# Optimization experiments

Measured on AMD Instinct MI355X. Metric: run time of the kernel, lower is better.

The kernel has to match this reference:

```python
import jax, jax.numpy as jnp
import numpy as np

N_HEAD = 50000
N_TAIL = 50000
E = 800000
F_IN = 256
D = 64
H = 4
FE = 64
N_ETYPES = 5
NEG_SLOPE = 0.2


def setup_inputs() -> dict:
    key = jax.random.key(0)
    ks = jax.random.split(key, 10)
    head_feature = jax.random.normal(ks[0], (N_HEAD, F_IN), jnp.float32)
    tail_feature = jax.random.normal(ks[1], (N_TAIL, F_IN), jnp.float32)
    head_ind = jax.random.randint(ks[2], (E,), 0, N_HEAD)
    tail_ind = jax.random.randint(ks[3], (E,), 0, N_TAIL)
    edge_list = jnp.stack([head_ind, tail_ind], axis=0)  # [2, E]
    tmp_edge = jax.random.randint(ks[4], (E,), 0, N_ETYPES)
    s = 0.05  # small init scale, mimics uniform(-stdv, stdv)
    W = jax.random.normal(ks[5], (F_IN, D * H), jnp.float32) * s
    W_e = jax.random.normal(ks[6], (FE, FE * H), jnp.float32) * s
    edge_emb = jax.random.normal(ks[7], (N_ETYPES, FE), jnp.float32) * s
    a_l = jax.random.normal(ks[8], (1, H, D), jnp.float32) * s
    a_r = jax.random.normal(jax.random.fold_in(ks[8], 1), (1, H, D), jnp.float32) * s
    a_e = jax.random.normal(ks[9], (1, H, FE), jnp.float32) * s
    return {
        "head_feature": head_feature,
        "tail_feature": tail_feature,
        "edge_list": edge_list,
        "tmp_edge": tmp_edge,
        "W": W,
        "W_e": W_e,
        "edge_emb": edge_emb,
        "a_l": a_l,
        "a_r": a_r,
        "a_e": a_e,
    }


def _layer(head_feature, tail_feature, head_ind, tail_ind, tmp_edge,
           W, W_e, edge_emb, a_l, a_r, a_e):
    n_head = head_feature.shape[0]
    # dense projections (dropout = identity in eval)
    h_head = (head_feature @ W).reshape(-1, H, D)      # [N_h, H, D]
    h_tail = (tail_feature @ W).reshape(-1, H, D)      # [N_t, H, D]
    e = (edge_emb @ W_e).reshape(-1, H, FE)            # [T, H, FE]
    # per-edge attention logits
    h_l = (a_l * h_head).sum(-1)[head_ind]             # [E, H]
    h_r = (a_r * h_tail).sum(-1)[tail_ind]             # [E, H]
    h_e = (a_e * e).sum(-1)[tmp_edge]                  # [E, H]
    score = jax.nn.leaky_relu(h_l + h_r + h_e, NEG_SLOPE)
    # segment softmax over edges grouped by destination (head) node, per head
    m = jax.ops.segment_max(score, head_ind, num_segments=n_head)   # [N_h, H]
    ex = jnp.exp(score - m[head_ind])                               # [E, H]
    z = jax.ops.segment_sum(ex, head_ind, num_segments=n_head)      # [N_h, H]
    alpha = ex / z[head_ind]                                        # [E, H]
    # weighted aggregation: sparse-mm per head, vectorized over heads
    msg = alpha[:, :, None] * h_tail[tail_ind]                      # [E, H, D]
    out = jax.ops.segment_sum(msg, head_ind, num_segments=n_head)   # [N_h, H, D]
    out = out.reshape(n_head, H * D)
    return jax.nn.elu(out)


def reference(head_feature, tail_feature, edge_list, tmp_edge,
              W, W_e, edge_emb, a_l, a_r, a_e):
    head_ind = edge_list[0]
    tail_ind = edge_list[1]
    return _layer(head_feature, tail_feature, head_ind, tail_ind, tmp_edge,
                  W, W_e, edge_emb, a_l, a_r, a_e)
```

## Files before the change

kernel.cpp:

```cpp
#include <hip/hip_runtime.h>
#include <hip/hip_bf16.h>
#include <math.h>

#define N_HEADN 50000
#define N_TAILN 50000
#define NE      800000
#define F_IN    256
#define HH      4
#define HD      256
#define FE      64
#define N_ETYPES 5
#define NEG_SLOPE 0.2f
#define NB_SCAN ((N_HEADN + 255) / 256)
#define NB_CVT  ((N_TAILN * F_IN) / (256 * 16))

typedef __attribute__((ext_vector_type(8))) short bf16x8;
typedef __attribute__((ext_vector_type(4))) float f32x4;

static __device__ __forceinline__ unsigned short f2bf(float f) {
    unsigned u = __float_as_uint(f);
    return (unsigned short)((u + 0x7FFF + ((u >> 16) & 1)) >> 16);
}
static __device__ __forceinline__ float bf2f(unsigned short u) {
    return __uint_as_float((unsigned)u << 16);
}

__global__ __launch_bounds__(256) void prep_kernel(const float* __restrict__ X,
                                                   unsigned short* __restrict__ Xb,
                                                   const float* __restrict__ W,
                                                   const float* __restrict__ a_l,
                                                   const float* __restrict__ W_e,
                                                   const float* __restrict__ a_e,
                                                   const float* __restrict__ edge_emb,
                                                   float* __restrict__ waT,
                                                   float* __restrict__ heo,
                                                   short* __restrict__ Wt,
                                                   int* __restrict__ counts) {
    const int b = blockIdx.x;
    if (b < NB_CVT) {
        size_t t = (size_t)b * 256 + threadIdx.x;
        const float4* xp = (const float4*)X + t * 4;
        float4 v0 = xp[0], v1 = xp[1], v2 = xp[2], v3 = xp[3];
        bf16x8 o0, o1;
        o0[0] = (short)f2bf(v0.x); o0[1] = (short)f2bf(v0.y);
        o0[2] = (short)f2bf(v0.z); o0[3] = (short)f2bf(v0.w);
        o0[4] = (short)f2bf(v1.x); o0[5] = (short)f2bf(v1.y);
        o0[6] = (short)f2bf(v1.z); o0[7] = (short)f2bf(v1.w);
        o1[0] = (short)f2bf(v2.x); o1[1] = (short)f2bf(v2.y);
        o1[2] = (short)f2bf(v2.z); o1[3] = (short)f2bf(v2.w);
        o1[4] = (short)f2bf(v3.x); o1[5] = (short)f2bf(v3.y);
        o1[6] = (short)f2bf(v3.z); o1[7] = (short)f2bf(v3.w);
        bf16x8* op = (bf16x8*)(Xb + t * 16);
        op[0] = o0;
        op[1] = o1;
    } else if (b == NB_CVT) {
        int k = threadIdx.x;
        #pragma unroll
        for (int h = 0; h < HH; ++h) {
            float s = 0.f;
            for (int d = 0; d < 64; ++d) s += a_l[h * 64 + d] * W[(size_t)k * HD + h * 64 + d];
            waT[h * 256 + k] = s;
        }
    } else if (b == NB_CVT + 1) {
        __shared__ float wae[FE][HH];
        int t = threadIdx.x;
        int k = t >> 2, h = t & 3;
        float s = 0.f;
        for (int f = 0; f < 64; ++f) s += a_e[h * 64 + f] * W_e[(size_t)k * (FE * HH) + h * 64 + f];
        wae[k][h] = s;
        __syncthreads();
        if (t < N_ETYPES * HH) {
            int ty = t >> 2, hh = t & 3;
            float acc = 0.f;
            for (int kk = 0; kk < FE; ++kk) acc += edge_emb[ty * FE + kk] * wae[kk][hh];
            heo[ty * HH + hh] = acc;
        }
    } else if (b < NB_CVT + 2 + 256) {
        int n = b - (NB_CVT + 2), k = threadIdx.x;
        Wt[(size_t)n * 256 + k] = (short)f2bf(W[(size_t)k * 256 + n]);
    } else {
        int j = (b - (NB_CVT + 258)) * 256 + threadIdx.x;
        if (j < N_HEADN) counts[j] = 0;
    }
}

__global__ void hist_kernel(const int* __restrict__ head, int* __restrict__ counts) {
    int e = blockIdx.x * 256 + threadIdx.x;
    atomicAdd(&counts[head[e]], 1);
}

__global__ void blocksum_kernel(const int* __restrict__ counts, int* __restrict__ blockSums) {
    __shared__ int s[256];
    int t = threadIdx.x, j = blockIdx.x * 256 + t;
    s[t] = (j < N_HEADN) ? counts[j] : 0;
    __syncthreads();
    for (int off = 128; off > 0; off >>= 1) {
        if (t < off) s[t] += s[t + off];
        __syncthreads();
    }
    if (t == 0) blockSums[blockIdx.x] = s[0];
}

__global__ void blockscan_kernel(const int* __restrict__ blockSums, int* __restrict__ blockOff) {
    __shared__ int s[256];
    int t = threadIdx.x;
    int v = (t < NB_SCAN) ? blockSums[t] : 0;
    s[t] = v;
    __syncthreads();
    for (int off = 1; off < 256; off <<= 1) {
        int u = (t >= off) ? s[t - off] : 0;
        __syncthreads();
        s[t] += u;
        __syncthreads();
    }
    if (t < NB_SCAN) blockOff[t] = s[t] - v;
}

__global__ void rowstart_kernel(const int* __restrict__ counts, const int* __restrict__ blockOff,
                                int* __restrict__ row_start, int* __restrict__ cursor) {
    __shared__ int s[256];
    int t = threadIdx.x, j = blockIdx.x * 256 + t;
    int c = (j < N_HEADN) ? counts[j] : 0;
    s[t] = c;
    __syncthreads();
    for (int off = 1; off < 256; off <<= 1) {
        int u = (t >= off) ? s[t - off] : 0;
        __syncthreads();
        s[t] += u;
        __syncthreads();
    }
    int excl = blockOff[blockIdx.x] + s[t] - c;
    if (j < N_HEADN) {
        row_start[j] = excl;
        cursor[j]    = excl;
        if (j == N_HEADN - 1) row_start[N_HEADN] = excl + c;
    }
}

__global__ __launch_bounds__(256) void head_dot_kernel(const float* __restrict__ X,
                                                       const float* __restrict__ waT,
                                                       float* __restrict__ hl) {
    const int wave = threadIdx.x >> 6;
    const int lane = threadIdx.x & 63;
    const int n = blockIdx.x * 4 + wave;
    float4 x = ((const float4*)(X + (size_t)n * F_IN))[lane];
    float p[HH];
    #pragma unroll
    for (int h = 0; h < HH; ++h) {
        float4 w = ((const float4*)(waT + h * 256))[lane];
        p[h] = x.x * w.x + x.y * w.y + x.z * w.z + x.w * w.w;
    }
    #pragma unroll
    for (int off = 1; off < 64; off <<= 1) {
        #pragma unroll
        for (int h = 0; h < HH; ++h) p[h] += __shfl_xor(p[h], off);
    }
    if (lane < HH) hl[(size_t)n * HH + lane] = p[lane];
}

__global__ __launch_bounds__(256) void proj_mfma_kernel(const unsigned short* __restrict__ Xb,
                                                        const short* __restrict__ Wt,
                                                        const float* __restrict__ a,
                                                        unsigned short* __restrict__ h_out,
                                                        float* __restrict__ dot_out,
                                                        int N) {
    const int tid  = threadIdx.x;
    const int w    = tid >> 6;
    const int lane = tid & 63;
    const int quad = lane >> 4;
    const int l15  = lane & 15;
    const int n0   = blockIdx.x * 64;

    int rbase[4];
    #pragma unroll
    for (int mt = 0; mt < 4; ++mt) {
        int r = n0 + mt * 16;
        rbase[mt] = (r + 16 <= N) ? r : (N - 16);
    }

    f32x4 acc[4][4];
    #pragma unroll
    for (int mt = 0; mt < 4; ++mt)
        #pragma unroll
        for (int ct = 0; ct < 4; ++ct)
            acc[mt][ct] = (f32x4){0.f, 0.f, 0.f, 0.f};

    const short* wbase = Wt + (size_t)(w * 64 + l15) * 256 + quad * 8;
    const unsigned short* xb[4];
    #pragma unroll
    for (int mt = 0; mt < 4; ++mt)
        xb[mt] = Xb + (size_t)(rbase[mt] + l15) * F_IN + quad * 8;

    #pragma unroll 2
    for (int k0 = 0; k0 < 256; k0 += 32) {
        bf16x8 af[4];
        #pragma unroll
        for (int mt = 0; mt < 4; ++mt) af[mt] = *(const bf16x8*)(xb[mt] + k0);
        #pragma unroll
        for (int ct = 0; ct < 4; ++ct) {
            bf16x8 bfrag = *(const bf16x8*)(wbase + (size_t)ct * 16 * 256 + k0);
            #pragma unroll
            for (int mt = 0; mt < 4; ++mt)
                acc[mt][ct] = __builtin_amdgcn_mfma_f32_16x16x32_bf16(af[mt], bfrag, acc[mt][ct], 0, 0, 0);
        }
    }

    float av[4];
    #pragma unroll
    for (int ct = 0; ct < 4; ++ct) av[ct] = a[w * 64 + ct * 16 + l15];

    #pragma unroll
    for (int mt = 0; mt < 4; ++mt) {
        #pragma unroll
        for (int ct = 0; ct < 4; ++ct) {
            #pragma unroll
            for (int r = 0; r < 4; ++r) {
                int row = rbase[mt] + quad * 4 + r;
                h_out[(size_t)row * HD + w * 64 + ct * 16 + l15] = f2bf(acc[mt][ct][r]);
            }
        }
        #pragma unroll
        for (int r = 0; r < 4; ++r) {
            float p = av[0] * acc[mt][0][r] + av[1] * acc[mt][1][r]
                    + av[2] * acc[mt][2][r] + av[3] * acc[mt][3][r];
            p += __shfl_xor(p, 1);
            p += __shfl_xor(p, 2);
            p += __shfl_xor(p, 4);
            p += __shfl_xor(p, 8);
            if (l15 == 0) {
                int row = rbase[mt] + quad * 4 + r;
                dot_out[(size_t)row * HH + w] = p;
            }
        }
    }
}

__global__ void scatter_kernel(const int* __restrict__ head, const int* __restrict__ tail,
                               const int* __restrict__ etype,
                               const float* __restrict__ hl, const float* __restrict__ hr,
                               const float* __restrict__ he,
                               int* __restrict__ cursor, int* __restrict__ packed,
                               float* __restrict__ exE) {
    int e = blockIdx.x * 256 + threadIdx.x;
    int h0 = head[e];
    int tl = tail[e];
    int ty = etype[e];
    float4 L = *(const float4*)(hl + (size_t)h0 * HH);
    float4 R = *(const float4*)(hr + (size_t)tl * HH);
    float4 T = *(const float4*)(he + ty * HH);
    float s0 = L.x + R.x + T.x;
    float s1 = L.y + R.y + T.y;
    float s2 = L.z + R.z + T.z;
    float s3 = L.w + R.w + T.w;
    s0 = (s0 > 0.f) ? s0 : NEG_SLOPE * s0;
    s1 = (s1 > 0.f) ? s1 : NEG_SLOPE * s1;
    s2 = (s2 > 0.f) ? s2 : NEG_SLOPE * s2;
    s3 = (s3 > 0.f) ? s3 : NEG_SLOPE * s3;
    float w0 = __expf(s0), w1 = __expf(s1), w2 = __expf(s2), w3 = __expf(s3);
    int pos = atomicAdd(&cursor[h0], 1);
    packed[pos] = tl;
    *(float4*)(exE + (size_t)pos * HH) = make_float4(w0, w1, w2, w3);
}

__global__ __launch_bounds__(256) void agg_kernel(const int* __restrict__ row_start,
                                                  const int* __restrict__ packed,
                                                  const float* __restrict__ exE,
                                                  const unsigned short* __restrict__ h_tail,
                                                  float* __restrict__ out) {
    const int wave = threadIdx.x >> 6;
    const int lane = threadIdx.x & 63;
    const int n = blockIdx.x * 4 + wave;
    const int s = row_start[n];
    const int e = row_start[n + 1];
    const int g = lane >> 4;
    const int q = lane & 15;
    const int h = q >> 2;

    float acc[16];
    #pragma unroll
    for (int c = 0; c < 16; ++c) acc[c] = 0.f;
    float z = 0.f;

    for (int base = s; base < e; base += 64) {
        const int cnt = (e - base < 64) ? (e - base) : 64;
        int myidx = 0;
        if (base + lane < e) myidx = packed[base + lane];
        #pragma unroll 4
        for (int i = 0; i < cnt; i += 4) {
            const int j = i + g;
            const int tl = __shfl(myidx, j);
            if (j < cnt) {
                const float w = exE[(size_t)(base + j) * HH + h];
                const uint4* p = (const uint4*)(h_tail + (size_t)tl * HD + q * 16);
                uint4 u0 = p[0];
                uint4 u1 = p[1];
                #pragma unroll
                for (int jj = 0; jj < 4; ++jj) {
                    unsigned u = ((const unsigned*)&u0)[jj];
                    acc[2 * jj]     += w * __uint_as_float(u << 16);
                    acc[2 * jj + 1] += w * __uint_as_float(u & 0xFFFF0000u);
                }
                #pragma unroll
                for (int jj = 0; jj < 4; ++jj) {
                    unsigned u = ((const unsigned*)&u1)[jj];
                    acc[8 + 2 * jj]     += w * __uint_as_float(u << 16);
                    acc[8 + 2 * jj + 1] += w * __uint_as_float(u & 0xFFFF0000u);
                }
                z += w;
            }
        }
    }

    #pragma unroll
    for (int c = 0; c < 16; ++c) {
        acc[c] += __shfl_xor(acc[c], 16);
        acc[c] += __shfl_xor(acc[c], 32);
    }
    z += __shfl_xor(z, 16);
    z += __shfl_xor(z, 32);

    float4 o;
    if (z > 0.f) {
        o.x = acc[g * 4 + 0] / z;
        o.y = acc[g * 4 + 1] / z;
        o.z = acc[g * 4 + 2] / z;
        o.w = acc[g * 4 + 3] / z;
        o.x = (o.x > 0.f) ? o.x : expm1f(o.x);
        o.y = (o.y > 0.f) ? o.y : expm1f(o.y);
        o.z = (o.z > 0.f) ? o.z : expm1f(o.z);
        o.w = (o.w > 0.f) ? o.w : expm1f(o.w);
    } else {
        o = make_float4(0.f, 0.f, 0.f, 0.f);
    }
    ((float4*)(out + (size_t)n * HD))[q * 4 + g] = o;
}

extern "C" void kernel_launch(void* const* d_in, const int* in_sizes, int n_in,
                              void* d_out, int out_size, void* d_ws, size_t ws_size,
                              hipStream_t stream) {
    const float* head_feature = (const float*)d_in[0];
    const float* tail_feature = (const float*)d_in[1];
    const int*   edge_list    = (const int*)d_in[2];
    const int*   tmp_edge     = (const int*)d_in[3];
    const float* W            = (const float*)d_in[4];
    const float* W_e          = (const float*)d_in[5];
    const float* edge_emb     = (const float*)d_in[6];
    const float* a_l          = (const float*)d_in[7];
    const float* a_r          = (const float*)d_in[8];
    const float* a_e          = (const float*)d_in[9];
    const int* head_ind = edge_list;
    const int* tail_ind = edge_list + NE;

    char* ws = (char*)d_ws;
    unsigned short* h_tail = (unsigned short*)ws; ws += sizeof(unsigned short) * (size_t)N_TAILN * HD;
    unsigned short* Xb = (unsigned short*)ws;
    float* exE    = (float*)(void*)Xb;
    int*   packed = (int*)(void*)((char*)(void*)Xb + sizeof(float) * (size_t)NE * HH);
    ws += sizeof(unsigned short) * (size_t)N_TAILN * HD;
    short* Wt        = (short*)ws; ws += sizeof(short) * 256 * 256;
    float* hl        = (float*)ws; ws += sizeof(float) * (size_t)N_HEADN * HH;
    float* hr        = (float*)ws; ws += sizeof(float) * (size_t)N_TAILN * HH;
    float* waT       = (float*)ws; ws += sizeof(float) * HH * 256;
    float* he        = (float*)ws; ws += sizeof(float) * 32;
    int*   counts    = (int*)ws;   ws += sizeof(int) * (size_t)N_HEADN;
    int*   row_start = (int*)ws;   ws += sizeof(int) * (size_t)(N_HEADN + 4);
    int*   cursor    = (int*)ws;   ws += sizeof(int) * (size_t)N_HEADN;
    int*   blockSums = (int*)ws;   ws += sizeof(int) * 256;
    int*   blockOff  = (int*)ws;   ws += sizeof(int) * 256;

    hipLaunchKernelGGL(prep_kernel, dim3(NB_CVT + 258 + NB_SCAN), dim3(256), 0, stream,
                       tail_feature, Xb, W, a_l, W_e, a_e, edge_emb, waT, he, Wt, counts);

    hipLaunchKernelGGL(hist_kernel, dim3(NE / 256), dim3(256), 0, stream,
                       head_ind, counts);
    hipLaunchKernelGGL(blocksum_kernel, dim3(NB_SCAN), dim3(256), 0, stream,
                       counts, blockSums);
    hipLaunchKernelGGL(blockscan_kernel, dim3(1), dim3(256), 0, stream,
                       blockSums, blockOff);
    hipLaunchKernelGGL(rowstart_kernel, dim3(NB_SCAN), dim3(256), 0, stream,
                       counts, blockOff, row_start, cursor);

    hipLaunchKernelGGL(head_dot_kernel, dim3(N_HEADN / 4), dim3(256), 0, stream,
                       head_feature, waT, hl);
    hipLaunchKernelGGL(proj_mfma_kernel, dim3((N_TAILN + 63) / 64), dim3(256), 0, stream,
                       Xb, Wt, a_r, h_tail, hr, N_TAILN);

    hipLaunchKernelGGL(scatter_kernel, dim3(NE / 256), dim3(256), 0, stream,
                       head_ind, tail_ind, tmp_edge, hl, hr, he, cursor, packed, exE);

    hipLaunchKernelGGL(agg_kernel, dim3(N_HEADN / 4), dim3(256), 0, stream,
                       row_start, packed, exE, h_tail, (float*)d_out);
}
```

Before: 360.2 us.

## Merge histogram into prep, fuse head-dot with projection, retile aggregation lanes

The histogram atomics move into the prep kernel, and counts are now zeroed with a memset instead of extra prep blocks. The head-dot kernel and the MFMA projection are merged into one launch so the two independent workloads share the GPU. The aggregation kernel now has 32 lanes per edge, each loading 16 bytes, and processes two edges per step where it used to process four, which halves accumulator registers and cross-lane reductions. This cuts launch count and gaps between kernels, but it adds a memset call and mixes blocks with very different register needs in one kernel, which may lower occupancy.

New measurement: 364.8 us. No clear change (+1.3%).

```diff
diff --git a/kernel.cpp b/kernel.cpp
--- a/kernel.cpp
+++ b/kernel.cpp
@@ -13,6 +13,8 @@
 #define NEG_SLOPE 0.2f
 #define NB_SCAN ((N_HEADN + 255) / 256)
 #define NB_CVT  ((N_TAILN * F_IN) / (256 * 16))
+#define NB_HIST (NE / 256)
+#define NB_PROJ ((N_TAILN + 63) / 64)
 
 typedef __attribute__((ext_vector_type(8))) short bf16x8;
 typedef __attribute__((ext_vector_type(4))) float f32x4;
@@ -25,7 +27,9 @@
     return __uint_as_float((unsigned)u << 16);
 }
 
-__global__ __launch_bounds__(256) void prep_kernel(const float* __restrict__ X,
+__global__ __launch_bounds__(256) void prep_kernel(const int* __restrict__ head,
+                                                   int* __restrict__ counts,
+                                                   const float* __restrict__ X,
                                                    unsigned short* __restrict__ Xb,
                                                    const float* __restrict__ W,
                                                    const float* __restrict__ a_l,
@@ -34,11 +38,13 @@
                                                    const float* __restrict__ edge_emb,
                                                    float* __restrict__ waT,
                                                    float* __restrict__ heo,
-                                                   short* __restrict__ Wt,
-                                                   int* __restrict__ counts) {
+                                                   short* __restrict__ Wt) {
     const int b = blockIdx.x;
-    if (b < NB_CVT) {
-        size_t t = (size_t)b * 256 + threadIdx.x;
+    if (b < NB_HIST) {
+        int e = b * 256 + threadIdx.x;
+        atomicAdd(&counts[head[e]], 1);
+    } else if (b < NB_HIST + NB_CVT) {
+        size_t t = (size_t)(b - NB_HIST) * 256 + threadIdx.x;
         const float4* xp = (const float4*)X + t * 4;
         float4 v0 = xp[0], v1 = xp[1], v2 = xp[2], v3 = xp[3];
         bf16x8 o0, o1;
@@ -53,7 +59,7 @@
         bf16x8* op = (bf16x8*)(Xb + t * 16);
         op[0] = o0;
         op[1] = o1;
-    } else if (b == NB_CVT) {
+    } else if (b == NB_HIST + NB_CVT) {
         int k = threadIdx.x;
         #pragma unroll
         for (int h = 0; h < HH; ++h) {
@@ -61,7 +67,7 @@
             for (int d = 0; d < 64; ++d) s += a_l[h * 64 + d] * W[(size_t)k * HD + h * 64 + d];
             waT[h * 256 + k] = s;
         }
-    } else if (b == NB_CVT + 1) {
+    } else if (b == NB_HIST + NB_CVT + 1) {
         __shared__ float wae[FE][HH];
         int t = threadIdx.x;
         int k = t >> 2, h = t & 3;
@@ -75,18 +81,10 @@
             for (int kk = 0; kk < FE; ++kk) acc += edge_emb[ty * FE + kk] * wae[kk][hh];
             heo[ty * HH + hh] = acc;
         }
-    } else if (b < NB_CVT + 2 + 256) {
-        int n = b - (NB_CVT + 2), k = threadIdx.x;
+    } else {
+        int n = b - (NB_HIST + NB_CVT + 2), k = threadIdx.x;
         Wt[(size_t)n * 256 + k] = (short)f2bf(W[(size_t)k * 256 + n]);
-    } else {
-        int j = (b - (NB_CVT + 258)) * 256 + threadIdx.x;
-        if (j < N_HEADN) counts[j] = 0;
-    }
-}
-
-__global__ void hist_kernel(const int* __restrict__ head, int* __restrict__ counts) {
-    int e = blockIdx.x * 256 + threadIdx.x;
-    atomicAdd(&counts[head[e]], 1);
+    }
 }
 
 __global__ void blocksum_kernel(const int* __restrict__ counts, int* __restrict__ blockSums) {
@@ -137,101 +135,102 @@
     }
 }
 
-__global__ __launch_bounds__(256) void head_dot_kernel(const float* __restrict__ X,
-                                                       const float* __restrict__ waT,
-                                                       float* __restrict__ hl) {
-    const int wave = threadIdx.x >> 6;
-    const int lane = threadIdx.x & 63;
-    const int n = blockIdx.x * 4 + wave;
-    float4 x = ((const float4*)(X + (size_t)n * F_IN))[lane];
-    float p[HH];
-    #pragma unroll
-    for (int h = 0; h < HH; ++h) {
-        float4 w = ((const float4*)(waT + h * 256))[lane];
-        p[h] = x.x * w.x + x.y * w.y + x.z * w.z + x.w * w.w;
-    }
-    #pragma unroll
-    for (int off = 1; off < 64; off <<= 1) {
-        #pragma unroll
-        for (int h = 0; h < HH; ++h) p[h] += __shfl_xor(p[h], off);
-    }
-    if (lane < HH) hl[(size_t)n * HH + lane] = p[lane];
-}
-
-__global__ __launch_bounds__(256) void proj_mfma_kernel(const unsigned short* __restrict__ Xb,
-                                                        const short* __restrict__ Wt,
-                                                        const float* __restrict__ a,
-                                                        unsigned short* __restrict__ h_out,
-                                                        float* __restrict__ dot_out,
-                                                        int N) {
-    const int tid  = threadIdx.x;
-    const int w    = tid >> 6;
-    const int lane = tid & 63;
-    const int quad = lane >> 4;
-    const int l15  = lane & 15;
-    const int n0   = blockIdx.x * 64;
-
-    int rbase[4];
-    #pragma unroll
-    for (int mt = 0; mt < 4; ++mt) {
-        int r = n0 + mt * 16;
-        rbase[mt] = (r + 16 <= N) ? r : (N - 16);
-    }
-
-    f32x4 acc[4][4];
-    #pragma unroll
-    for (int mt = 0; mt < 4; ++mt)
-        #pragma unroll
-        for (int ct = 0; ct < 4; ++ct)
-            acc[mt][ct] = (f32x4){0.f, 0.f, 0.f, 0.f};
-
-    const short* wbase = Wt + (size_t)(w * 64 + l15) * 256 + quad * 8;
-    const unsigned short* xb[4];
-    #pragma unroll
-    for (int mt = 0; mt < 4; ++mt)
-        xb[mt] = Xb + (size_t)(rbase[mt] + l15) * F_IN + quad * 8;
-
-    #pragma unroll 2
-    for (int k0 = 0; k0 < 256; k0 += 32) {
-        bf16x8 af[4];
-        #pragma unroll
-        for (int mt = 0; mt < 4; ++mt) af[mt] = *(const bf16x8*)(xb[mt] + k0);
-        #pragma unroll
-        for (int ct = 0; ct < 4; ++ct) {
-            bf16x8 bfrag = *(const bf16x8*)(wbase + (size_t)ct * 16 * 256 + k0);
-            #pragma unroll
-            for (int mt = 0; mt < 4; ++mt)
-                acc[mt][ct] = __builtin_amdgcn_mfma_f32_16x16x32_bf16(af[mt], bfrag, acc[mt][ct], 0, 0, 0);
-        }
-    }
-
-    float av[4];
-    #pragma unroll
-    for (int ct = 0; ct < 4; ++ct) av[ct] = a[w * 64 + ct * 16 + l15];
-
-    #pragma unroll
-    for (int mt = 0; mt < 4; ++mt) {
-        #pragma unroll
-        for (int ct = 0; ct < 4; ++ct) {
+__global__ __launch_bounds__(256) void hd_proj_kernel(const float* __restrict__ Xh,
+                                                      const float* __restrict__ waT,
+                                                      float* __restrict__ hl,
+                                                      const unsigned short* __restrict__ Xb,
+                                                      const short* __restrict__ Wt,
+                                                      const float* __restrict__ a,
+                                                      unsigned short* __restrict__ h_out,
+                                                      float* __restrict__ dot_out,
+                                                      int N) {
+    if (blockIdx.x < NB_PROJ) {
+        const int tid  = threadIdx.x;
+        const int w    = tid >> 6;
+        const int lane = tid & 63;
+        const int quad = lane >> 4;
+        const int l15  = lane & 15;
+        const int n0   = blockIdx.x * 64;
+
+        int rbase[4];
+        #pragma unroll
+        for (int mt = 0; mt < 4; ++mt) {
+            int r = n0 + mt * 16;
+            rbase[mt] = (r + 16 <= N) ? r : (N - 16);
+        }
+
+        f32x4 acc[4][4];
+        #pragma unroll
+        for (int mt = 0; mt < 4; ++mt)
+            #pragma unroll
+            for (int ct = 0; ct < 4; ++ct)
+                acc[mt][ct] = (f32x4){0.f, 0.f, 0.f, 0.f};
+
+        const short* wbase = Wt + (size_t)(w * 64 + l15) * 256 + quad * 8;
+        const unsigned short* xb[4];
+        #pragma unroll
+        for (int mt = 0; mt < 4; ++mt)
+            xb[mt] = Xb + (size_t)(rbase[mt] + l15) * F_IN + quad * 8;
+
+        #pragma unroll 2
+        for (int k0 = 0; k0 < 256; k0 += 32) {
+            bf16x8 af[4];
+            #pragma unroll
+            for (int mt = 0; mt < 4; ++mt) af[mt] = *(const bf16x8*)(xb[mt] + k0);
+            #pragma unroll
+            for (int ct = 0; ct < 4; ++ct) {
+                bf16x8 bfrag = *(const bf16x8*)(wbase + (size_t)ct * 16 * 256 + k0);
+                #pragma unroll
+                for (int mt = 0; mt < 4; ++mt)
+                    acc[mt][ct] = __builtin_amdgcn_mfma_f32_16x16x32_bf16(af[mt], bfrag, acc[mt][ct], 0, 0, 0);
+            }
+        }
+
+        float av[4];
+        #pragma unroll
+        for (int ct = 0; ct < 4; ++ct) av[ct] = a[w * 64 + ct * 16 + l15];
+
+        #pragma unroll
+        for (int mt = 0; mt < 4; ++mt) {
+            #pragma unroll
+            for (int ct = 0; ct < 4; ++ct) {
+                #pragma unroll
+                for (int r = 0; r < 4; ++r) {
+                    int row = rbase[mt] + quad * 4 + r;
+                    h_out[(size_t)row * HD + w * 64 + ct * 16 + l15] = f2bf(acc[mt][ct][r]);
+                }
+            }
             #pragma unroll
             for (int r = 0; r < 4; ++r) {
-                int row = rbase[mt] + quad * 4 + r;
-                h_out[(size_t)row * HD + w * 64 + ct * 16 + l15] = f2bf(acc[mt][ct][r]);
+                float p = av[0] * acc[mt][0][r] + av[1] * acc[mt][1][r]
+                        + av[2] * acc[mt][2][r] + av[3] * acc[mt][3][r];
+                p += __shfl_xor(p, 1);
+                p += __shfl_xor(p, 2);
+                p += __shfl_xor(p, 4);
+                p += __shfl_xor(p, 8);
+                if (l15 == 0) {
+                    int row = rbase[mt] + quad * 4 + r;
+                    dot_out[(size_t)row * HH + w] = p;
+                }
             }
         }
-        #pragma unroll
-        for (int r = 0; r < 4; ++r) {
-            float p = av[0] * acc[mt][0][r] + av[1] * acc[mt][1][r]
-                    + av[2] * acc[mt][2][r] + av[3] * acc[mt][3][r];
-            p += __shfl_xor(p, 1);
-            p += __shfl_xor(p, 2);
-            p += __shfl_xor(p, 4);
-            p += __shfl_xor(p, 8);
-            if (l15 == 0) {
-                int row = rbase[mt] + quad * 4 + r;
-                dot_out[(size_t)row * HH + w] = p;
-            }
-        }
+    } else {
+        const int wave = threadIdx.x >> 6;
+        const int lane = threadIdx.x & 63;
+        const int n = (blockIdx.x - NB_PROJ) * 4 + wave;
+        float4 x = ((const float4*)(Xh + (size_t)n * F_IN))[lane];
+        float p[HH];
+        #pragma unroll
+        for (int h = 0; h < HH; ++h) {
+            float4 w = ((const float4*)(waT + h * 256))[lane];
+            p[h] = x.x * w.x + x.y * w.y + x.z * w.z + x.w * w.w;
+        }
+        #pragma unroll
+        for (int off = 1; off < 64; off <<= 1) {
+            #pragma unroll
+            for (int h = 0; h < HH; ++h) p[h] += __shfl_xor(p[h], off);
+        }
+        if (lane < HH) hl[(size_t)n * HH + lane] = p[lane];
     }
 }
 
@@ -272,39 +271,31 @@
     const int n = blockIdx.x * 4 + wave;
     const int s = row_start[n];
     const int e = row_start[n + 1];
-    const int g = lane >> 4;
-    const int q = lane & 15;
-    const int h = q >> 2;
-
-    float acc[16];
+    const int g = lane >> 5;
+    const int q = lane & 31;
+    const int h = q >> 3;
+
+    float acc[8];
     #pragma unroll
-    for (int c = 0; c < 16; ++c) acc[c] = 0.f;
+    for (int c = 0; c < 8; ++c) acc[c] = 0.f;
     float z = 0.f;
 
     for (int base = s; base < e; base += 64) {
         const int cnt = (e - base < 64) ? (e - base) : 64;
         int myidx = 0;
         if (base + lane < e) myidx = packed[base + lane];
-        #pragma unroll 4
-        for (int i = 0; i < cnt; i += 4) {
+        #pragma unroll 8
+        for (int i = 0; i < cnt; i += 2) {
             const int j = i + g;
             const int tl = __shfl(myidx, j);
             if (j < cnt) {
                 const float w = exE[(size_t)(base + j) * HH + h];
-                const uint4* p = (const uint4*)(h_tail + (size_t)tl * HD + q * 16);
-                uint4 u0 = p[0];
-                uint4 u1 = p[1];
+                uint4 u = *(const uint4*)(h_tail + (size_t)tl * HD + q * 8);
                 #pragma unroll
-                for (int jj = 0; jj < 4; ++jj) {
-                    unsigned u = ((const unsigned*)&u0)[jj];
-                    acc[2 * jj]     += w * __uint_as_float(u << 16);
-                    acc[2 * jj + 1] += w * __uint_as_float(u & 0xFFFF0000u);
-                }
-                #pragma unroll
-                for (int jj = 0; jj < 4; ++jj) {
-                    unsigned u = ((const unsigned*)&u1)[jj];
-                    acc[8 + 2 * jj]     += w * __uint_as_float(u << 16);
-                    acc[8 + 2 * jj + 1] += w * __uint_as_float(u & 0xFFFF0000u);
+                for (int d = 0; d < 4; ++d) {
+                    unsigned uu = ((const unsigned*)&u)[d];
+                    acc[2 * d]     += w * __uint_as_float(uu << 16);
+                    acc[2 * d + 1] += w * __uint_as_float(uu & 0xFFFF0000u);
                 }
                 z += w;
             }
@@ -312,19 +303,15 @@
     }
 
     #pragma unroll
-    for (int c = 0; c < 16; ++c) {
-        acc[c] += __shfl_xor(acc[c], 16);
-        acc[c] += __shfl_xor(acc[c], 32);
-    }
-    z += __shfl_xor(z, 16);
+    for (int c = 0; c < 8; ++c) acc[c] += __shfl_xor(acc[c], 32);
     z += __shfl_xor(z, 32);
 
     float4 o;
     if (z > 0.f) {
-        o.x = acc[g * 4 + 0] / z;
-        o.y = acc[g * 4 + 1] / z;
-        o.z = acc[g * 4 + 2] / z;
-        o.w = acc[g * 4 + 3] / z;
+        o.x = acc[4 * g + 0] / z;
+        o.y = acc[4 * g + 1] / z;
+        o.z = acc[4 * g + 2] / z;
+        o.w = acc[4 * g + 3] / z;
         o.x = (o.x > 0.f) ? o.x : expm1f(o.x);
         o.y = (o.y > 0.f) ? o.y : expm1f(o.y);
         o.z = (o.z > 0.f) ? o.z : expm1f(o.z);
@@ -332,7 +319,7 @@
     } else {
         o = make_float4(0.f, 0.f, 0.f, 0.f);
     }
-    ((float4*)(out + (size_t)n * HD))[q * 4 + g] = o;
+    ((float4*)(out + (size_t)n * HD))[q * 2 + g] = o;
 }
 
 extern "C" void kernel_launch(void* const* d_in, const int* in_sizes, int n_in,
@@ -368,11 +355,12 @@
     int*   blockSums = (int*)ws;   ws += sizeof(int) * 256;
     int*   blockOff  = (int*)ws;   ws += sizeof(int) * 256;
 
-    hipLaunchKernelGGL(prep_kernel, dim3(NB_CVT + 258 + NB_SCAN), dim3(256), 0, stream,
-                       tail_feature, Xb, W, a_l, W_e, a_e, edge_emb, waT, he, Wt, counts);
-
-    hipLaunchKernelGGL(hist_kernel, dim3(NE / 256), dim3(256), 0, stream,
-                       head_ind, counts);
+    hipMemsetAsync(counts, 0, sizeof(int) * (size_t)N_HEADN, stream);
+
+    hipLaunchKernelGGL(prep_kernel, dim3(NB_HIST + NB_CVT + 258), dim3(256), 0, stream,
+                       head_ind, counts, tail_feature, Xb,
+                       W, a_l, W_e, a_e, edge_emb, waT, he, Wt);
+
     hipLaunchKernelGGL(blocksum_kernel, dim3(NB_SCAN), dim3(256), 0, stream,
                        counts, blockSums);
     hipLaunchKernelGGL(blockscan_kernel, dim3(1), dim3(256), 0, stream,
@@ -380,9 +368,8 @@
     hipLaunchKernelGGL(rowstart_kernel, dim3(NB_SCAN), dim3(256), 0, stream,
                        counts, blockOff, row_start, cursor);
 
-    hipLaunchKernelGGL(head_dot_kernel, dim3(N_HEADN / 4), dim3(256), 0, stream,
-                       head_feature, waT, hl);
-    hipLaunchKernelGGL(proj_mfma_kernel, dim3((N_TAILN + 63) / 64), dim3(256), 0, stream,
+    hipLaunchKernelGGL(hd_proj_kernel, dim3(NB_PROJ + N_HEADN / 4), dim3(256), 0, stream,
+                       head_feature, waT, hl,
                        Xb, Wt, a_r, h_tail, hr, N_TAILN);
 
     hipLaunchKernelGGL(scatter_kernel, dim3(NE / 256), dim3(256), 0, stream,
```
